# Optimization experiments

Measured on AMD Instinct MI355X. Metric: run time of the kernel, lower is better.

The kernel has to match this reference:

```python
import jax, jax.numpy as jnp
import numpy as np

B, S, D, H, P = 4, 512, 512, 8, 16
DK = D // H  # 64


def setup_inputs() -> dict:
    k0 = jax.random.key(0)
    ks = jax.random.split(k0, 10)
    std = 0.02
    lin = lambda k, shape: jax.random.normal(k, shape, dtype=jnp.float32) * std
    inp = {}
    inp["query"] = jax.random.normal(ks[0], (B, S, D), dtype=jnp.float32)
    inp["key"] = jax.random.normal(ks[1], (B, S, D), dtype=jnp.float32)
    inp["value"] = jax.random.normal(ks[2], (B, S, D), dtype=jnp.float32)
    inp["Wq"] = lin(ks[3], (D, D)); inp["bq"] = jnp.zeros((D,), jnp.float32)
    inp["Wk"] = lin(ks[4], (D, D)); inp["bk"] = jnp.zeros((D,), jnp.float32)
    inp["Wv"] = lin(ks[5], (D, D)); inp["bv"] = jnp.zeros((D,), jnp.float32)
    inp["Wo"] = lin(ks[6], (D, D)); inp["bo"] = jnp.zeros((D,), jnp.float32)
    inp["rel_table"] = lin(ks[7], (2 * P + 1, DK))  # nn.Embedding(2P+1, d_k)
    inp["gamma"] = jnp.ones((D,), jnp.float32)
    inp["beta"] = jnp.zeros((D,), jnp.float32)
    inp["mask"] = jnp.ones((B, S), dtype=jnp.int32)
    inp["relative_positions"] = jax.random.randint(ks[8], (B, S, S, DK), -32, 33, dtype=jnp.int32)
    return inp


def reference(query, key, value, Wq, bq, Wk, bk, Wv, bv, Wo, bo, rel_table, gamma, beta, mask, relative_positions):
    b, s, d = query.shape
    dk = rel_table.shape[1]
    h = d // dk
    pmax = (rel_table.shape[0] - 1) // 2

    def heads(x, W, bias):
        return (x @ W.T + bias).reshape(b, s, h, dk).transpose(0, 2, 1, 3)  # [b,h,s,dk]

    Q = heads(query, Wq, bq)
    K = heads(key, Wk, bk)
    V = heads(value, Wv, bv)

    scores = jnp.einsum('bhid,bhjd->bhij', Q, K) / jnp.sqrt(jnp.float32(dk))

    # torch: einsum('bhid,bijde->bhije', Q, emb(idx)).mean(-1)
    # mean over e commutes with the d-contraction -> pre-average the table.
    idx = jnp.clip(relative_positions, -pmax, pmax) + pmax  # [b,i,j,d]
    bias_d = rel_table.mean(axis=-1)[idx]                   # [b,i,j,d]
    scores = scores + jnp.einsum('bhid,bijd->bhij', Q, bias_d)

    scores = jnp.where(mask[:, None, None, :] == 0, jnp.float32(-1e9), scores)
    attn = jax.nn.softmax(scores, axis=-1)  # dropout is identity in eval

    ctx = jnp.einsum('bhij,bhjd->bhid', attn, V).transpose(0, 2, 1, 3).reshape(b, s, d)
    out = ctx @ Wo.T + bo

    x = out + query  # residual
    mu = x.mean(-1, keepdims=True)
    var = x.var(-1, keepdims=True)
    y = (x - mu) / jnp.sqrt(var + 1e-5) * gamma + beta
    return (y, attn)
```

## Files before the change

kernel.cpp:

```cpp
#include <hip/hip_runtime.h>
#include <hip/hip_bf16.h>

#define BB 4
#define SS 512
#define DD 512
#define HH 8
#define DK 64
#define PP 16
#define TSZ 33

typedef __bf16 bf16x8 __attribute__((ext_vector_type(8)));
typedef __bf16 bf16x4 __attribute__((ext_vector_type(4)));
typedef float  f32x4  __attribute__((ext_vector_type(4)));

union U8 { bf16x8 v; int u[4]; };

__device__ inline bf16x8 cvt8(const float* __restrict__ p) {
    f32x4 a = *(const f32x4*)p;
    f32x4 b = *(const f32x4*)(p + 4);
    bf16x8 r;
    r[0] = (__bf16)a[0]; r[1] = (__bf16)a[1]; r[2] = (__bf16)a[2]; r[3] = (__bf16)a[3];
    r[4] = (__bf16)b[0]; r[5] = (__bf16)b[1]; r[6] = (__bf16)b[2]; r[7] = (__bf16)b[3];
    return r;
}

__global__ void tmean_kernel(const float* __restrict__ rel_table, float* __restrict__ Tm) {
    int t = threadIdx.x;
    if (t < TSZ) {
        float s = 0.f;
        for (int e = 0; e < DK; ++e) s += rel_table[t * DK + e];
        Tm[t] = s * (1.f / DK);
    }
}

__global__ void proj_mfma_kernel(const float* __restrict__ X0, const float* __restrict__ X1,
                                 const float* __restrict__ X2,
                                 const float* __restrict__ W0, const float* __restrict__ W1,
                                 const float* __restrict__ W2,
                                 const float* __restrict__ B0, const float* __restrict__ B1,
                                 const float* __restrict__ B2,
                                 __bf16* __restrict__ O0, __bf16* __restrict__ O1,
                                 __bf16* __restrict__ O2) {
    int z = blockIdx.z;
    const float* X = (z == 0) ? X0 : (z == 1) ? X1 : X2;
    const float* W = (z == 0) ? W0 : (z == 1) ? W1 : W2;
    const float* bias = (z == 0) ? B0 : (z == 1) ? B1 : B2;
    __bf16* out = (z == 0) ? O0 : (z == 1) ? O1 : O2;
    int mode = (z == 2);

    int lane = threadIdx.x, wave = threadIdx.y;
    int tm = blockIdx.y * 4 + wave;
    int tn = blockIdx.x;
    int m = lane & 15, quad = lane >> 4;

    const float* arow = X + (size_t)(tm * 16 + m) * DD + quad * 8;
    const float* brow = W + (size_t)(tn * 16 + m) * DD + quad * 8;

    f32x4 acc = {0.f, 0.f, 0.f, 0.f};
    for (int k0 = 0; k0 < DD; k0 += 32) {
        bf16x8 a = cvt8(arow + k0);
        bf16x8 b = cvt8(brow + k0);
        acc = __builtin_amdgcn_mfma_f32_16x16x32_bf16(a, b, acc, 0, 0, 0);
    }

    int col = tn * 16 + m;
    int h = col >> 6, dk = col & (DK - 1);
    float bv = bias[col];
#pragma unroll
    for (int r = 0; r < 4; ++r) {
        int rowg = tm * 16 + quad * 4 + r;
        int b = rowg >> 9, i = rowg & (SS - 1);
        float v = acc[r] + bv;
        if (mode == 0)
            out[((size_t)(b * HH + h) * SS + i) * DK + dk] = (__bf16)v;
        else
            out[((size_t)(b * HH + h) * DK + dk) * SS + i] = (__bf16)v;
    }
}

__launch_bounds__(512, 2)
__global__ void f1_kernel(const __bf16* __restrict__ Qbf, const __bf16* __restrict__ Kbf,
                          const int* __restrict__ relpos, const float* __restrict__ Tm,
                          const int* __restrict__ mask, float* __restrict__ attn,
                          float* __restrict__ pm, float* __restrict__ pl) {
    __shared__ float bias_sh[8 * 16 * 132];

    int l = threadIdx.x, w = threadIdx.y;
    int jq = blockIdx.x, i0 = blockIdx.y, b = blockIdx.z;
    int m = l & 15, quad = l >> 4;

    float tmf = Tm[l < TSZ ? l : 0];
    int tmb = (int)__builtin_bit_cast(unsigned short, (__bf16)tmf);

    {
        const int ISTR = SS * DK;
        const int* rbase = relpos + ((size_t)(b * SS + i0 * 16) * SS + jq * 128 + w * 16 + m) * DK + quad * 8;
        int4 u0 = *(const int4*)(rbase);
        int4 u1 = *(const int4*)(rbase + 4);
        int4 u2 = *(const int4*)(rbase + 32);
        int4 u3 = *(const int4*)(rbase + 36);
        for (int i = 0; i < 16; ++i) {
            int4 n0, n1, n2, n3;
            if (i < 15) {
                const int* nb = rbase + (i + 1) * ISTR;
                n0 = *(const int4*)(nb);
                n1 = *(const int4*)(nb + 4);
                n2 = *(const int4*)(nb + 32);
                n3 = *(const int4*)(nb + 36);
            }
            const __bf16* qp = Qbf + ((size_t)(b * HH + (m & 7)) * SS + i0 * 16 + i) * DK + quad * 8;
            bf16x8 A0 = *(const bf16x8*)qp;
            bf16x8 A1 = *(const bf16x8*)(qp + 32);
#define LUT(vv) __builtin_amdgcn_ds_bpermute((min(max((vv), -PP), PP) + PP) << 2, tmb)
            U8 Bf0, Bf1;
            Bf0.u[0] = LUT(u0.x) | (LUT(u0.y) << 16);
            Bf0.u[1] = LUT(u0.z) | (LUT(u0.w) << 16);
            Bf0.u[2] = LUT(u1.x) | (LUT(u1.y) << 16);
            Bf0.u[3] = LUT(u1.z) | (LUT(u1.w) << 16);
            Bf1.u[0] = LUT(u2.x) | (LUT(u2.y) << 16);
            Bf1.u[1] = LUT(u2.z) | (LUT(u2.w) << 16);
            Bf1.u[2] = LUT(u3.x) | (LUT(u3.y) << 16);
            Bf1.u[3] = LUT(u3.z) | (LUT(u3.w) << 16);
#undef LUT
            f32x4 accB = {0.f, 0.f, 0.f, 0.f};
            accB = __builtin_amdgcn_mfma_f32_16x16x32_bf16(A0, Bf0.v, accB, 0, 0, 0);
            accB = __builtin_amdgcn_mfma_f32_16x16x32_bf16(A1, Bf1.v, accB, 0, 0, 0);
            if (quad < 2) {
#pragma unroll
                for (int r = 0; r < 4; ++r) {
                    int h = quad * 4 + r;
                    bias_sh[h * 2112 + i * 132 + w * 16 + m] = accB[r];
                }
            }
            u0 = n0; u1 = n1; u2 = n2; u3 = n3;
        }
    }

    const __bf16* qrow = Qbf + ((size_t)(b * HH + w) * SS + i0 * 16 + m) * DK + quad * 8;
    bf16x8 a0 = *(const bf16x8*)qrow;
    bf16x8 a1 = *(const bf16x8*)(qrow + 32);

    f32x4 acc[8];
#pragma unroll
    for (int jt = 0; jt < 8; ++jt) {
        const __bf16* krow = Kbf + ((size_t)(b * HH + w) * SS + jq * 128 + jt * 16 + m) * DK + quad * 8;
        bf16x8 b0 = *(const bf16x8*)krow;
        bf16x8 b1 = *(const bf16x8*)(krow + 32);
        f32x4 c = {0.f, 0.f, 0.f, 0.f};
        c = __builtin_amdgcn_mfma_f32_16x16x32_bf16(a0, b0, c, 0, 0, 0);
        c = __builtin_amdgcn_mfma_f32_16x16x32_bf16(a1, b1, c, 0, 0, 0);
        acc[jt] = c;
    }

    __syncthreads();

#pragma unroll
    for (int jt = 0; jt < 8; ++jt) {
#pragma unroll
        for (int r = 0; r < 4; ++r) {
            float bv = bias_sh[w * 2112 + (quad * 4 + r) * 132 + jt * 16 + m];
            acc[jt][r] = acc[jt][r] * 0.125f + bv;
        }
    }

#pragma unroll
    for (int jt = 0; jt < 8; ++jt) {
        int mv = mask[b * SS + jq * 128 + jt * 16 + m];
        if (mv == 0) {
#pragma unroll
            for (int r = 0; r < 4; ++r) acc[jt][r] = -1e9f;
        }
    }

#pragma unroll
    for (int r = 0; r < 4; ++r) {
        float mx = -1e30f;
#pragma unroll
        for (int jt = 0; jt < 8; ++jt) mx = fmaxf(mx, acc[jt][r]);
        mx = fmaxf(mx, __shfl_xor(mx, 1));
        mx = fmaxf(mx, __shfl_xor(mx, 2));
        mx = fmaxf(mx, __shfl_xor(mx, 4));
        mx = fmaxf(mx, __shfl_xor(mx, 8));
        float sum = 0.f;
#pragma unroll
        for (int jt = 0; jt < 8; ++jt) {
            float e = __expf(acc[jt][r] - mx);
            acc[jt][r] = e;
            sum += e;
        }
        sum += __shfl_xor(sum, 1);
        sum += __shfl_xor(sum, 2);
        sum += __shfl_xor(sum, 4);
        sum += __shfl_xor(sum, 8);
        if (m == 0) {
            int row = i0 * 16 + quad * 4 + r;
            pm[((size_t)(b * HH + w) * SS + row) * 4 + jq] = mx;
            pl[((size_t)(b * HH + w) * SS + row) * 4 + jq] = sum;
        }
    }

#pragma unroll
    for (int jt = 0; jt < 8; ++jt) {
#pragma unroll
        for (int r = 0; r < 4; ++r) {
            attn[((size_t)(b * HH + w) * SS + i0 * 16 + quad * 4 + r) * SS
                 + jq * 128 + jt * 16 + m] = acc[jt][r];
        }
    }
}

__launch_bounds__(256, 4)
__global__ void f2_kernel(float* __restrict__ attn, const float* __restrict__ pm,
                          const float* __restrict__ pl, const __bf16* __restrict__ Vt,
                          __bf16* __restrict__ ctx_bsd) {
    __shared__ float scl[4][16];
    __shared__ __bf16 p_sh[16 * 520];

    int t = threadIdx.x;
    int l = t & 63, wv = t >> 6;
    int i0 = blockIdx.x, bh = blockIdx.y;

    if (t < 16) {
        int row = i0 * 16 + t;
        float m0 = pm[((size_t)bh * SS + row) * 4 + 0];
        float m1 = pm[((size_t)bh * SS + row) * 4 + 1];
        float m2 = pm[((size_t)bh * SS + row) * 4 + 2];
        float m3 = pm[((size_t)bh * SS + row) * 4 + 3];
        float l0 = pl[((size_t)bh * SS + row) * 4 + 0];
        float l1 = pl[((size_t)bh * SS + row) * 4 + 1];
        float l2 = pl[((size_t)bh * SS + row) * 4 + 2];
        float l3 = pl[((size_t)bh * SS + row) * 4 + 3];
        float M = fmaxf(fmaxf(m0, m1), fmaxf(m2, m3));
        float e0 = __expf(m0 - M), e1 = __expf(m1 - M);
        float e2 = __expf(m2 - M), e3 = __expf(m3 - M);
        float L = l0 * e0 + l1 * e1 + l2 * e2 + l3 * e3;
        float inv = 1.f / L;
        scl[0][t] = e0 * inv; scl[1][t] = e1 * inv;
        scl[2][t] = e2 * inv; scl[3][t] = e3 * inv;
    }
    __syncthreads();

    float* arow = attn + ((size_t)bh * SS + i0 * 16) * SS;
#pragma unroll
    for (int rr = 0; rr < 4; ++rr) {
        int row = wv * 4 + rr;
#pragma unroll
        for (int it = 0; it < 2; ++it) {
            int col = it * 256 + l * 4;
            f32x4 v = *(f32x4*)(arow + (size_t)row * SS + col);
            float s = scl[col >> 7][row];
            v[0] *= s; v[1] *= s; v[2] *= s; v[3] *= s;
            *(f32x4*)(arow + (size_t)row * SS + col) = v;
            bf16x4 pk = {(__bf16)v[0], (__bf16)v[1], (__bf16)v[2], (__bf16)v[3]};
            *(bf16x4*)&p_sh[row * 520 + col] = pk;
        }
    }
    __syncthreads();

    int m = l & 15, quad = l >> 4;
    f32x4 acc = {0.f, 0.f, 0.f, 0.f};
    const __bf16* vrow = Vt + ((size_t)bh * DK + wv * 16 + m) * SS + quad * 8;
    for (int k0 = 0; k0 < SS; k0 += 32) {
        bf16x8 aF = *(bf16x8*)&p_sh[m * 520 + k0 + quad * 8];
        bf16x8 bF = *(const bf16x8*)(vrow + k0);
        acc = __builtin_amdgcn_mfma_f32_16x16x32_bf16(aF, bF, acc, 0, 0, 0);
    }
    int b = bh >> 3, h = bh & 7;
#pragma unroll
    for (int r = 0; r < 4; ++r) {
        ctx_bsd[((size_t)(b * SS + i0 * 16 + quad * 4 + r)) * DD + h * DK + wv * 16 + m]
            = (__bf16)acc[r];
    }
}

__global__ void outproj_mfma_kernel(const __bf16* __restrict__ Xc, const float* __restrict__ Wo,
                                    const float* __restrict__ bo, const float* __restrict__ query,
                                    float* __restrict__ xres) {
    int lane = threadIdx.x, wave = threadIdx.y;
    int tm = blockIdx.y * 4 + wave;
    int tn = blockIdx.x;
    int m = lane & 15, quad = lane >> 4;

    const __bf16* arow = Xc + (size_t)(tm * 16 + m) * DD + quad * 8;
    const float*  brow = Wo + (size_t)(tn * 16 + m) * DD + quad * 8;

    f32x4 acc = {0.f, 0.f, 0.f, 0.f};
    for (int k0 = 0; k0 < DD; k0 += 32) {
        bf16x8 a = *(const bf16x8*)(arow + k0);
        bf16x8 b = cvt8(brow + k0);
        acc = __builtin_amdgcn_mfma_f32_16x16x32_bf16(a, b, acc, 0, 0, 0);
    }

    int col = tn * 16 + m;
    float bv = bo[col];
#pragma unroll
    for (int r = 0; r < 4; ++r) {
        int rowg = tm * 16 + quad * 4 + r;
        xres[(size_t)rowg * DD + col] = acc[r] + bv + query[(size_t)rowg * DD + col];
    }
}

__global__ void ln_kernel(const float* __restrict__ x, const float* __restrict__ gamma,
                          const float* __restrict__ beta, float* __restrict__ y) {
    int r = blockIdx.x;
    int t = threadIdx.x;
    float v0 = x[r * DD + t];
    float v1 = x[r * DD + t + 256];
    __shared__ float red[4];
    float s = v0 + v1;
#pragma unroll
    for (int off = 32; off >= 1; off >>= 1) s += __shfl_xor(s, off);
    if ((t & 63) == 0) red[t >> 6] = s;
    __syncthreads();
    float mu = (red[0] + red[1] + red[2] + red[3]) * (1.f / DD);
    __syncthreads();
    float d0 = v0 - mu, d1 = v1 - mu;
    float sq = d0 * d0 + d1 * d1;
#pragma unroll
    for (int off = 32; off >= 1; off >>= 1) sq += __shfl_xor(sq, off);
    if ((t & 63) == 0) red[t >> 6] = sq;
    __syncthreads();
    float var = (red[0] + red[1] + red[2] + red[3]) * (1.f / DD);
    float inv = rsqrtf(var + 1e-5f);
    y[r * DD + t] = d0 * inv * gamma[t] + beta[t];
    y[r * DD + t + 256] = d1 * inv * gamma[t + 256] + beta[t + 256];
}

extern "C" void kernel_launch(void* const* d_in, const int* in_sizes, int n_in,
                              void* d_out, int out_size, void* d_ws, size_t ws_size,
                              hipStream_t stream) {
    const float* query  = (const float*)d_in[0];
    const float* key    = (const float*)d_in[1];
    const float* value  = (const float*)d_in[2];
    const float* Wq     = (const float*)d_in[3];
    const float* bq     = (const float*)d_in[4];
    const float* Wk     = (const float*)d_in[5];
    const float* bk     = (const float*)d_in[6];
    const float* Wv     = (const float*)d_in[7];
    const float* bv     = (const float*)d_in[8];
    const float* Wo     = (const float*)d_in[9];
    const float* bo     = (const float*)d_in[10];
    const float* rtab   = (const float*)d_in[11];
    const float* gamma  = (const float*)d_in[12];
    const float* beta   = (const float*)d_in[13];
    const int*   mask   = (const int*)d_in[14];
    const int*   relpos = (const int*)d_in[15];

    float* out = (float*)d_out;
    float* y    = out;
    float* attn = out + (size_t)BB * SS * DD;

    char* wsb = (char*)d_ws;
    float*  Tm    = (float*)wsb;   wsb += 256;
    __bf16* Qbf   = (__bf16*)wsb;  wsb += (size_t)BB * HH * SS * DK * 2;
    __bf16* Kbf   = (__bf16*)wsb;  wsb += (size_t)BB * HH * SS * DK * 2;
    __bf16* Vtbf  = (__bf16*)wsb;  wsb += (size_t)BB * HH * DK * SS * 2;
    __bf16* ctxbf = (__bf16*)wsb;  wsb += (size_t)BB * SS * DD * 2;
    float*  xres  = (float*)wsb;   wsb += (size_t)BB * SS * DD * 4;
    float*  pm    = (float*)wsb;   wsb += (size_t)BB * HH * SS * 4 * 4;
    float*  pl    = (float*)wsb;   wsb += (size_t)BB * HH * SS * 4 * 4;

    hipLaunchKernelGGL(tmean_kernel, dim3(1), dim3(64), 0, stream, rtab, Tm);

    dim3 wblk(64, 4);
    hipLaunchKernelGGL(proj_mfma_kernel, dim3(DD / 16, (BB * SS) / 64, 3), wblk, 0, stream,
                       query, key, value, Wq, Wk, Wv, bq, bk, bv, Qbf, Kbf, Vtbf);

    hipLaunchKernelGGL(f1_kernel, dim3(4, SS / 16, BB), dim3(64, 8), 0, stream,
                       Qbf, Kbf, relpos, Tm, mask, attn, pm, pl);

    hipLaunchKernelGGL(f2_kernel, dim3(SS / 16, BB * HH), dim3(256), 0, stream,
                       attn, pm, pl, Vtbf, ctxbf);

    hipLaunchKernelGGL(outproj_mfma_kernel, dim3(DD / 16, (BB * SS) / 64), wblk, 0, stream,
                       ctxbf, Wo, bo, query, xres);

    hipLaunchKernelGGL(ln_kernel, dim3(BB * SS), dim3(256), 0, stream, xres, gamma, beta, y);
}
```

Measured before the change: 538.8 us.

## Fuse full-row softmax into score kernel and out-projection with layernorm

The score kernel now handles 8 query rows across the full key length per block. It finishes the softmax in place and writes normalized attention directly, which drops the partial max/sum buffers and the rescale-and-rewrite pass in the second kernel. The table-mean kernel and a bf16 conversion of Wo are folded into the projection launch. Out-projection, residual and layernorm are fused into one kernel that keeps rows in LDS, removing a global round trip and a launch. The bias tile is stored as bf16 to fit in LDS, which costs precision. Half of the MFMA output lanes are wasted with only 8 rows per tile.

Result: no change. 543.8 us (+0.9%).

```diff
diff --git a/kernel.cpp b/kernel.cpp
--- a/kernel.cpp
+++ b/kernel.cpp
@@ -24,31 +24,36 @@
     return r;
 }
 
-__global__ void tmean_kernel(const float* __restrict__ rel_table, float* __restrict__ Tm) {
-    int t = threadIdx.x;
-    if (t < TSZ) {
-        float s = 0.f;
-        for (int e = 0; e < DK; ++e) s += rel_table[t * DK + e];
-        Tm[t] = s * (1.f / DK);
-    }
-}
-
-__global__ void proj_mfma_kernel(const float* __restrict__ X0, const float* __restrict__ X1,
-                                 const float* __restrict__ X2,
-                                 const float* __restrict__ W0, const float* __restrict__ W1,
-                                 const float* __restrict__ W2,
-                                 const float* __restrict__ B0, const float* __restrict__ B1,
-                                 const float* __restrict__ B2,
-                                 __bf16* __restrict__ O0, __bf16* __restrict__ O1,
-                                 __bf16* __restrict__ O2) {
+__global__ void prep_kernel(const float* __restrict__ X0, const float* __restrict__ X1,
+                            const float* __restrict__ X2,
+                            const float* __restrict__ W0, const float* __restrict__ W1,
+                            const float* __restrict__ W2,
+                            const float* __restrict__ B0, const float* __restrict__ B1,
+                            const float* __restrict__ B2,
+                            __bf16* __restrict__ O0, __bf16* __restrict__ O1,
+                            __bf16* __restrict__ O2,
+                            const float* __restrict__ Wo, __bf16* __restrict__ Wo_bf,
+                            const float* __restrict__ rel_table, float* __restrict__ Tm) {
     int z = blockIdx.z;
+    int lane = threadIdx.x, wave = threadIdx.y;
+    if (z == 3) {
+        int bid = blockIdx.y * 32 + blockIdx.x;
+        int t = wave * 64 + lane;
+        int idx = bid * 256 + t;
+        Wo_bf[idx] = (__bf16)Wo[idx];
+        if (bid == 0 && t < TSZ) {
+            float s = 0.f;
+            for (int e = 0; e < DK; ++e) s += rel_table[t * DK + e];
+            Tm[t] = s * (1.f / DK);
+        }
+        return;
+    }
     const float* X = (z == 0) ? X0 : (z == 1) ? X1 : X2;
     const float* W = (z == 0) ? W0 : (z == 1) ? W1 : W2;
     const float* bias = (z == 0) ? B0 : (z == 1) ? B1 : B2;
     __bf16* out = (z == 0) ? O0 : (z == 1) ? O1 : O2;
     int mode = (z == 2);
 
-    int lane = threadIdx.x, wave = threadIdx.y;
     int tm = blockIdx.y * 4 + wave;
     int tn = blockIdx.x;
     int m = lane & 15, quad = lane >> 4;
@@ -81,34 +86,35 @@
 __launch_bounds__(512, 2)
 __global__ void f1_kernel(const __bf16* __restrict__ Qbf, const __bf16* __restrict__ Kbf,
                           const int* __restrict__ relpos, const float* __restrict__ Tm,
-                          const int* __restrict__ mask, float* __restrict__ attn,
-                          float* __restrict__ pm, float* __restrict__ pl) {
-    __shared__ float bias_sh[8 * 16 * 132];
+                          const int* __restrict__ mask, float* __restrict__ attn) {
+    __shared__ __bf16 bias_sh[8 * 8 * 520];
 
     int l = threadIdx.x, w = threadIdx.y;
-    int jq = blockIdx.x, i0 = blockIdx.y, b = blockIdx.z;
+    int i0 = blockIdx.x, b = blockIdx.y;
+    int I0 = i0 * 8;
     int m = l & 15, quad = l >> 4;
 
     float tmf = Tm[l < TSZ ? l : 0];
     int tmb = (int)__builtin_bit_cast(unsigned short, (__bf16)tmf);
 
     {
-        const int ISTR = SS * DK;
-        const int* rbase = relpos + ((size_t)(b * SS + i0 * 16) * SS + jq * 128 + w * 16 + m) * DK + quad * 8;
-        int4 u0 = *(const int4*)(rbase);
-        int4 u1 = *(const int4*)(rbase + 4);
-        int4 u2 = *(const int4*)(rbase + 32);
-        int4 u3 = *(const int4*)(rbase + 36);
-        for (int i = 0; i < 16; ++i) {
+        const int* p0 = relpos + ((size_t)(b * SS + I0) * SS + (w * 4) * 16 + m) * DK + quad * 8;
+        int4 u0 = *(const int4*)(p0);
+        int4 u1 = *(const int4*)(p0 + 4);
+        int4 u2 = *(const int4*)(p0 + 32);
+        int4 u3 = *(const int4*)(p0 + 36);
+        for (int unit = 0; unit < 32; ++unit) {
+            int tt = unit >> 3, i = unit & 7;
             int4 n0, n1, n2, n3;
-            if (i < 15) {
-                const int* nb = rbase + (i + 1) * ISTR;
-                n0 = *(const int4*)(nb);
-                n1 = *(const int4*)(nb + 4);
-                n2 = *(const int4*)(nb + 32);
-                n3 = *(const int4*)(nb + 36);
+            if (unit < 31) {
+                int t2 = (unit + 1) >> 3, i2 = (unit + 1) & 7;
+                const int* np = relpos + ((size_t)(b * SS + I0 + i2) * SS + (w * 4 + t2) * 16 + m) * DK + quad * 8;
+                n0 = *(const int4*)(np);
+                n1 = *(const int4*)(np + 4);
+                n2 = *(const int4*)(np + 32);
+                n3 = *(const int4*)(np + 36);
             }
-            const __bf16* qp = Qbf + ((size_t)(b * HH + (m & 7)) * SS + i0 * 16 + i) * DK + quad * 8;
+            const __bf16* qp = Qbf + ((size_t)(b * HH + (m & 7)) * SS + I0 + i) * DK + quad * 8;
             bf16x8 A0 = *(const bf16x8*)qp;
             bf16x8 A1 = *(const bf16x8*)(qp + 32);
 #define LUT(vv) __builtin_amdgcn_ds_bpermute((min(max((vv), -PP), PP) + PP) << 2, tmb)
@@ -129,21 +135,21 @@
 #pragma unroll
                 for (int r = 0; r < 4; ++r) {
                     int h = quad * 4 + r;
-                    bias_sh[h * 2112 + i * 132 + w * 16 + m] = accB[r];
+                    bias_sh[(h * 8 + i) * 520 + w * 64 + tt * 16 + m] = (__bf16)accB[r];
                 }
             }
             u0 = n0; u1 = n1; u2 = n2; u3 = n3;
         }
     }
 
-    const __bf16* qrow = Qbf + ((size_t)(b * HH + w) * SS + i0 * 16 + m) * DK + quad * 8;
+    const __bf16* qrow = Qbf + ((size_t)(b * HH + w) * SS + I0 + (m & 7)) * DK + quad * 8;
     bf16x8 a0 = *(const bf16x8*)qrow;
     bf16x8 a1 = *(const bf16x8*)(qrow + 32);
 
-    f32x4 acc[8];
-#pragma unroll
-    for (int jt = 0; jt < 8; ++jt) {
-        const __bf16* krow = Kbf + ((size_t)(b * HH + w) * SS + jq * 128 + jt * 16 + m) * DK + quad * 8;
+    f32x4 acc[32];
+#pragma unroll
+    for (int jt = 0; jt < 32; ++jt) {
+        const __bf16* krow = Kbf + ((size_t)(b * HH + w) * SS + jt * 16 + m) * DK + quad * 8;
         bf16x8 b0 = *(const bf16x8*)krow;
         bf16x8 b1 = *(const bf16x8*)(krow + 32);
         f32x4 c = {0.f, 0.f, 0.f, 0.f};
@@ -154,36 +160,31 @@
 
     __syncthreads();
 
-#pragma unroll
-    for (int jt = 0; jt < 8; ++jt) {
+    int iLDS = (quad & 1) * 4;
+#pragma unroll
+    for (int jt = 0; jt < 32; ++jt) {
+        int mv = mask[b * SS + jt * 16 + m];
 #pragma unroll
         for (int r = 0; r < 4; ++r) {
-            float bv = bias_sh[w * 2112 + (quad * 4 + r) * 132 + jt * 16 + m];
-            acc[jt][r] = acc[jt][r] * 0.125f + bv;
-        }
-    }
-
-#pragma unroll
-    for (int jt = 0; jt < 8; ++jt) {
-        int mv = mask[b * SS + jq * 128 + jt * 16 + m];
-        if (mv == 0) {
-#pragma unroll
-            for (int r = 0; r < 4; ++r) acc[jt][r] = -1e9f;
-        }
-    }
-
+            float bv = (float)bias_sh[(w * 8 + iLDS + r) * 520 + jt * 16 + m];
+            float v = acc[jt][r] * 0.125f + bv;
+            acc[jt][r] = (mv == 0) ? -1e9f : v;
+        }
+    }
+
+    float inv[4];
 #pragma unroll
     for (int r = 0; r < 4; ++r) {
         float mx = -1e30f;
 #pragma unroll
-        for (int jt = 0; jt < 8; ++jt) mx = fmaxf(mx, acc[jt][r]);
+        for (int jt = 0; jt < 32; ++jt) mx = fmaxf(mx, acc[jt][r]);
         mx = fmaxf(mx, __shfl_xor(mx, 1));
         mx = fmaxf(mx, __shfl_xor(mx, 2));
         mx = fmaxf(mx, __shfl_xor(mx, 4));
         mx = fmaxf(mx, __shfl_xor(mx, 8));
         float sum = 0.f;
 #pragma unroll
-        for (int jt = 0; jt < 8; ++jt) {
+        for (int jt = 0; jt < 32; ++jt) {
             float e = __expf(acc[jt][r] - mx);
             acc[jt][r] = e;
             sum += e;
@@ -192,65 +193,38 @@
         sum += __shfl_xor(sum, 2);
         sum += __shfl_xor(sum, 4);
         sum += __shfl_xor(sum, 8);
-        if (m == 0) {
-            int row = i0 * 16 + quad * 4 + r;
-            pm[((size_t)(b * HH + w) * SS + row) * 4 + jq] = mx;
-            pl[((size_t)(b * HH + w) * SS + row) * 4 + jq] = sum;
-        }
-    }
-
-#pragma unroll
-    for (int jt = 0; jt < 8; ++jt) {
-#pragma unroll
-        for (int r = 0; r < 4; ++r) {
-            attn[((size_t)(b * HH + w) * SS + i0 * 16 + quad * 4 + r) * SS
-                 + jq * 128 + jt * 16 + m] = acc[jt][r];
+        inv[r] = 1.f / sum;
+    }
+
+    if (quad < 2) {
+#pragma unroll
+        for (int jt = 0; jt < 32; ++jt) {
+#pragma unroll
+            for (int r = 0; r < 4; ++r) {
+                attn[((size_t)(b * HH + w) * SS + I0 + quad * 4 + r) * SS + jt * 16 + m]
+                    = acc[jt][r] * inv[r];
+            }
         }
     }
 }
 
 __launch_bounds__(256, 4)
-__global__ void f2_kernel(float* __restrict__ attn, const float* __restrict__ pm,
-                          const float* __restrict__ pl, const __bf16* __restrict__ Vt,
+__global__ void f2_kernel(const float* __restrict__ attn, const __bf16* __restrict__ Vt,
                           __bf16* __restrict__ ctx_bsd) {
-    __shared__ float scl[4][16];
     __shared__ __bf16 p_sh[16 * 520];
 
     int t = threadIdx.x;
     int l = t & 63, wv = t >> 6;
     int i0 = blockIdx.x, bh = blockIdx.y;
 
-    if (t < 16) {
-        int row = i0 * 16 + t;
-        float m0 = pm[((size_t)bh * SS + row) * 4 + 0];
-        float m1 = pm[((size_t)bh * SS + row) * 4 + 1];
-        float m2 = pm[((size_t)bh * SS + row) * 4 + 2];
-        float m3 = pm[((size_t)bh * SS + row) * 4 + 3];
-        float l0 = pl[((size_t)bh * SS + row) * 4 + 0];
-        float l1 = pl[((size_t)bh * SS + row) * 4 + 1];
-        float l2 = pl[((size_t)bh * SS + row) * 4 + 2];
-        float l3 = pl[((size_t)bh * SS + row) * 4 + 3];
-        float M = fmaxf(fmaxf(m0, m1), fmaxf(m2, m3));
-        float e0 = __expf(m0 - M), e1 = __expf(m1 - M);
-        float e2 = __expf(m2 - M), e3 = __expf(m3 - M);
-        float L = l0 * e0 + l1 * e1 + l2 * e2 + l3 * e3;
-        float inv = 1.f / L;
-        scl[0][t] = e0 * inv; scl[1][t] = e1 * inv;
-        scl[2][t] = e2 * inv; scl[3][t] = e3 * inv;
-    }
-    __syncthreads();
-
-    float* arow = attn + ((size_t)bh * SS + i0 * 16) * SS;
+    const float* arow = attn + ((size_t)bh * SS + i0 * 16) * SS;
 #pragma unroll
     for (int rr = 0; rr < 4; ++rr) {
         int row = wv * 4 + rr;
 #pragma unroll
         for (int it = 0; it < 2; ++it) {
             int col = it * 256 + l * 4;
-            f32x4 v = *(f32x4*)(arow + (size_t)row * SS + col);
-            float s = scl[col >> 7][row];
-            v[0] *= s; v[1] *= s; v[2] *= s; v[3] *= s;
-            *(f32x4*)(arow + (size_t)row * SS + col) = v;
+            f32x4 v = *(const f32x4*)(arow + (size_t)row * SS + col);
             bf16x4 pk = {(__bf16)v[0], (__bf16)v[1], (__bf16)v[2], (__bf16)v[3]};
             *(bf16x4*)&p_sh[row * 520 + col] = pk;
         }
@@ -273,57 +247,69 @@
     }
 }
 
-__global__ void outproj_mfma_kernel(const __bf16* __restrict__ Xc, const float* __restrict__ Wo,
-                                    const float* __restrict__ bo, const float* __restrict__ query,
-                                    float* __restrict__ xres) {
-    int lane = threadIdx.x, wave = threadIdx.y;
-    int tm = blockIdx.y * 4 + wave;
-    int tn = blockIdx.x;
-    int m = lane & 15, quad = lane >> 4;
-
-    const __bf16* arow = Xc + (size_t)(tm * 16 + m) * DD + quad * 8;
-    const float*  brow = Wo + (size_t)(tn * 16 + m) * DD + quad * 8;
-
-    f32x4 acc = {0.f, 0.f, 0.f, 0.f};
+__launch_bounds__(512, 2)
+__global__ void k4_kernel(const __bf16* __restrict__ Xc, const __bf16* __restrict__ Wo_bf,
+                          const float* __restrict__ bo, const float* __restrict__ query,
+                          const float* __restrict__ gamma, const float* __restrict__ beta,
+                          float* __restrict__ y) {
+    __shared__ float xs[16 * 520];
+
+    int l = threadIdx.x, w = threadIdx.y;
+    int rowb = blockIdx.x * 16;
+    int m = l & 15, quad = l >> 4;
+
+    f32x4 acc[4] = {{0,0,0,0},{0,0,0,0},{0,0,0,0},{0,0,0,0}};
     for (int k0 = 0; k0 < DD; k0 += 32) {
-        bf16x8 a = *(const bf16x8*)(arow + k0);
-        bf16x8 b = cvt8(brow + k0);
-        acc = __builtin_amdgcn_mfma_f32_16x16x32_bf16(a, b, acc, 0, 0, 0);
-    }
-
-    int col = tn * 16 + m;
-    float bv = bo[col];
-#pragma unroll
-    for (int r = 0; r < 4; ++r) {
-        int rowg = tm * 16 + quad * 4 + r;
-        xres[(size_t)rowg * DD + col] = acc[r] + bv + query[(size_t)rowg * DD + col];
-    }
-}
-
-__global__ void ln_kernel(const float* __restrict__ x, const float* __restrict__ gamma,
-                          const float* __restrict__ beta, float* __restrict__ y) {
-    int r = blockIdx.x;
-    int t = threadIdx.x;
-    float v0 = x[r * DD + t];
-    float v1 = x[r * DD + t + 256];
-    __shared__ float red[4];
-    float s = v0 + v1;
-#pragma unroll
-    for (int off = 32; off >= 1; off >>= 1) s += __shfl_xor(s, off);
-    if ((t & 63) == 0) red[t >> 6] = s;
+        bf16x8 a0 = *(const bf16x8*)(Xc + (size_t)(rowb + m) * DD + k0 + quad * 8);
+#pragma unroll
+        for (int tt = 0; tt < 4; ++tt) {
+            int nrow = (w * 4 + tt) * 16 + m;
+            bf16x8 b0 = *(const bf16x8*)(Wo_bf + (size_t)nrow * DD + k0 + quad * 8);
+            acc[tt] = __builtin_amdgcn_mfma_f32_16x16x32_bf16(a0, b0, acc[tt], 0, 0, 0);
+        }
+    }
+#pragma unroll
+    for (int tt = 0; tt < 4; ++tt) {
+        int col = (w * 4 + tt) * 16 + m;
+        float bv = bo[col];
+#pragma unroll
+        for (int r = 0; r < 4; ++r) {
+            int row = quad * 4 + r;
+            xs[row * 520 + col] = acc[tt][r] + bv + query[(size_t)(rowb + row) * DD + col];
+        }
+    }
     __syncthreads();
-    float mu = (red[0] + red[1] + red[2] + red[3]) * (1.f / DD);
-    __syncthreads();
-    float d0 = v0 - mu, d1 = v1 - mu;
-    float sq = d0 * d0 + d1 * d1;
-#pragma unroll
-    for (int off = 32; off >= 1; off >>= 1) sq += __shfl_xor(sq, off);
-    if ((t & 63) == 0) red[t >> 6] = sq;
-    __syncthreads();
-    float var = (red[0] + red[1] + red[2] + red[3]) * (1.f / DD);
-    float inv = rsqrtf(var + 1e-5f);
-    y[r * DD + t] = d0 * inv * gamma[t] + beta[t];
-    y[r * DD + t + 256] = d1 * inv * gamma[t + 256] + beta[t + 256];
+
+#pragma unroll
+    for (int rr = 0; rr < 2; ++rr) {
+        int row = w * 2 + rr;
+        float v[8];
+        *(f32x4*)(v) = *(f32x4*)&xs[row * 520 + l * 8];
+        *(f32x4*)(v + 4) = *(f32x4*)&xs[row * 520 + l * 8 + 4];
+        float s = 0.f;
+#pragma unroll
+        for (int e = 0; e < 8; ++e) s += v[e];
+#pragma unroll
+        for (int off = 32; off >= 1; off >>= 1) s += __shfl_xor(s, off);
+        float mu = s * (1.f / DD);
+        float sq = 0.f;
+#pragma unroll
+        for (int e = 0; e < 8; ++e) { v[e] -= mu; sq += v[e] * v[e]; }
+#pragma unroll
+        for (int off = 32; off >= 1; off >>= 1) sq += __shfl_xor(sq, off);
+        float invs = rsqrtf(sq * (1.f / DD) + 1e-5f);
+        f32x4 g0 = *(const f32x4*)(gamma + l * 8);
+        f32x4 g1 = *(const f32x4*)(gamma + l * 8 + 4);
+        f32x4 be0 = *(const f32x4*)(beta + l * 8);
+        f32x4 be1 = *(const f32x4*)(beta + l * 8 + 4);
+        f32x4 o0, o1;
+#pragma unroll
+        for (int e = 0; e < 4; ++e) o0[e] = v[e] * invs * g0[e] + be0[e];
+#pragma unroll
+        for (int e = 0; e < 4; ++e) o1[e] = v[e + 4] * invs * g1[e] + be1[e];
+        *(f32x4*)(y + (size_t)(rowb + row) * DD + l * 8) = o0;
+        *(f32x4*)(y + (size_t)(rowb + row) * DD + l * 8 + 4) = o1;
+    }
 }
 
 extern "C" void kernel_launch(void* const* d_in, const int* in_sizes, int n_in,
@@ -356,24 +342,19 @@
     __bf16* Kbf   = (__bf16*)wsb;  wsb += (size_t)BB * HH * SS * DK * 2;
     __bf16* Vtbf  = (__bf16*)wsb;  wsb += (size_t)BB * HH * DK * SS * 2;
     __bf16* ctxbf = (__bf16*)wsb;  wsb += (size_t)BB * SS * DD * 2;
-    float*  xres  = (float*)wsb;   wsb += (size_t)BB * SS * DD * 4;
-    float*  pm    = (float*)wsb;   wsb += (size_t)BB * HH * SS * 4 * 4;
-    float*  pl    = (float*)wsb;   wsb += (size_t)BB * HH * SS * 4 * 4;
-
-    hipLaunchKernelGGL(tmean_kernel, dim3(1), dim3(64), 0, stream, rtab, Tm);
+    __bf16* Wo_bf = (__bf16*)wsb;  wsb += (size_t)DD * DD * 2;
 
     dim3 wblk(64, 4);
-    hipLaunchKernelGGL(proj_mfma_kernel, dim3(DD / 16, (BB * SS) / 64, 3), wblk, 0, stream,
-                       query, key, value, Wq, Wk, Wv, bq, bk, bv, Qbf, Kbf, Vtbf);
-
-    hipLaunchKernelGGL(f1_kernel, dim3(4, SS / 16, BB), dim3(64, 8), 0, stream,
-                       Qbf, Kbf, relpos, Tm, mask, attn, pm, pl);
+    hipLaunchKernelGGL(prep_kernel, dim3(32, 32, 4), wblk, 0, stream,
+                       query, key, value, Wq, Wk, Wv, bq, bk, bv, Qbf, Kbf, Vtbf,
+                       Wo, Wo_bf, rtab, Tm);
+
+    hipLaunchKernelGGL(f1_kernel, dim3(SS / 8, BB), dim3(64, 8), 0, stream,
+                       Qbf, Kbf, relpos, Tm, mask, attn);
 
     hipLaunchKernelGGL(f2_kernel, dim3(SS / 16, BB * HH), dim3(256), 0, stream,
-                       attn, pm, pl, Vtbf, ctxbf);
-
-    hipLaunchKernelGGL(outproj_mfma_kernel, dim3(DD / 16, (BB * SS) / 64), wblk, 0, stream,
-                       ctxbf, Wo, bo, query, xres);
-
-    hipLaunchKernelGGL(ln_kernel, dim3(BB * SS), dim3(256), 0, stream, xres, gamma, beta, y);
-}
+                       attn, Vtbf, ctxbf);
+
+    hipLaunchKernelGGL(k4_kernel, dim3((BB * SS) / 16), dim3(64, 8), 0, stream,
+                       ctxbf, Wo_bf, bo, query, gamma, beta, y);
+}
```
